# Kernel optimization log

Measured on AMD Instinct MI355X. Metric: run time of the kernel, lower is better.

The kernel has to match this reference:

```python
import jax, jax.numpy as jnp
import numpy as np

E = 64        # num_experts
T = 65536     # num_tokens (sum of group_sizes)
D_IN = 512    # in_features
D_OUT = 512   # out_features


def setup_inputs() -> dict:
    key = jax.random.key(0)
    k1, k2, k3 = jax.random.split(key, 3)
    inputs = jax.random.normal(k1, (T, D_IN), dtype=jnp.float32)
    # lecun_normal init scale for kernel
    kernel = jax.random.normal(k2, (E, D_IN, D_OUT), dtype=jnp.float32) * (1.0 / np.sqrt(D_IN))
    bias = jax.random.normal(k3, (D_OUT,), dtype=jnp.float32) * 0.02
    # equal-size contiguous per-expert token groups, summing to T
    group_sizes = jnp.full((E,), T // E, dtype=jnp.int32)
    return {"inputs": inputs, "kernel": kernel, "bias": bias, "group_sizes": group_sizes}


def reference(inputs, kernel, bias, group_sizes):
    # Grouped (ragged) matmul: tokens are laid out contiguously by expert;
    # group_sizes[e] tokens are multiplied by kernel[e]. This is exactly
    # jax.lax.ragged_dot (megablocks-style grouped GEMM semantics).
    y = jax.lax.ragged_dot(inputs, kernel, group_sizes)  # [T, D_OUT]
    return y + bias[None, :]
```

## Files before the change

kernel.cpp:

```cpp
#include <hip/hip_runtime.h>
#include <hip/hip_bf16.h>

#define NUM_E 64
#define D_K 512
#define D_N 512
#define BM 128
#define BN 128
#define MAX_TILES 576
#define GRID_X (MAX_TILES * 4)

typedef __bf16 bf16x8 __attribute__((ext_vector_type(8)));
typedef float f32x16 __attribute__((ext_vector_type(16)));
typedef float f32x4 __attribute__((ext_vector_type(4)));
typedef unsigned int u32;
typedef unsigned short u16;

__device__ __forceinline__ int imin(int a, int b) { return a < b ? a : b; }

__device__ __forceinline__ void gll16(const void* g, void* l) {
    __builtin_amdgcn_global_load_lds(
        (const __attribute__((address_space(1))) u32*)(uintptr_t)g,
        (__attribute__((address_space(3))) u32*)(uintptr_t)l, 16, 0, 0);
}

__device__ __forceinline__ void cvt_split(float a, u32 &hi, u32 &lo) {
    u32 u  = __float_as_uint(a);
    u32 rh = (u + 0x7FFFu + ((u >> 16) & 1u)) & 0xFFFF0000u;
    hi = rh >> 16;
    float res = a - __uint_as_float(rh);
    lo = __float_as_uint(res) >> 16;
}

__global__ void build_tiles_kernel(const int* __restrict__ gs,
                                   int* __restrict__ cnt,
                                   int* __restrict__ desc) {
    int e = threadIdx.x;
    if (e >= NUM_E) return;
    int row = 0, toff = 0;
    for (int i = 0; i < e; ++i) {
        int g = gs[i];
        row += g;
        toff += (g + BM - 1) / BM;
    }
    int g = gs[e];
    int nt = (g + BM - 1) / BM;
    for (int i = 0; i < nt; ++i) {
        int b = 3 * (toff + i);
        desc[b]     = e;
        desc[b + 1] = row + i * BM;
        desc[b + 2] = imin(BM, g - i * BM);
    }
    if (e == NUM_E - 1) cnt[0] = toff + nt;
}

__global__ void convert_x_kernel(const float* __restrict__ X, u16* __restrict__ Xc,
                                 int nquads) {
    int idx = blockIdx.x * blockDim.x + threadIdx.x;
    int stride = gridDim.x * blockDim.x;
    for (int q = idx; q < nquads; q += stride) {
        int row = q >> 7;
        int c4  = (q & 127) * 4;
        f32x4 v = *(const f32x4*)(X + (size_t)q * 4);
        u32 h[4], l[4];
        #pragma unroll
        for (int j = 0; j < 4; ++j) cvt_split(v[j], h[j], l[j]);
        uint2 hp, lp;
        hp.x = h[0] | (h[1] << 16); hp.y = h[2] | (h[3] << 16);
        lp.x = l[0] | (l[1] << 16); lp.y = l[2] | (l[3] << 16);
        *(uint2*)(Xc + (size_t)row * 1024 + c4)       = hp;
        *(uint2*)(Xc + (size_t)row * 1024 + 512 + c4) = lp;
    }
}

__global__ void convert_w_kernel(const float* __restrict__ W, u16* __restrict__ Wc) {
    __shared__ u16 Thi[64 * 68];
    __shared__ u16 Tlo[64 * 68];
    int bid = blockIdx.x;
    int e  = bid >> 6;
    int ti = (bid >> 3) & 7;
    int tj = bid & 7;
    int tid = threadIdx.x;

    const float* Wp = W + (size_t)e * D_K * D_N;
    #pragma unroll
    for (int it = 0; it < 4; ++it) {
        int kl = it * 16 + (tid >> 4);
        int nl = (tid & 15) * 4;
        f32x4 v = *(const f32x4*)(Wp + (size_t)(ti * 64 + kl) * D_N + tj * 64 + nl);
        u32 h[4], l[4];
        #pragma unroll
        for (int j = 0; j < 4; ++j) cvt_split(v[j], h[j], l[j]);
        uint2 hp, lp;
        hp.x = h[0] | (h[1] << 16); hp.y = h[2] | (h[3] << 16);
        lp.x = l[0] | (l[1] << 16); lp.y = l[2] | (l[3] << 16);
        *(uint2*)(Thi + kl * 68 + nl) = hp;
        *(uint2*)(Tlo + kl * 68 + nl) = lp;
    }
    __syncthreads();
    #pragma unroll
    for (int it = 0; it < 4; ++it) {
        int nl = it * 16 + (tid >> 4);
        int kq = tid & 15;
        u32 h[4], l[4];
        #pragma unroll
        for (int j = 0; j < 4; ++j) {
            h[j] = Thi[(kq * 4 + j) * 68 + nl];
            l[j] = Tlo[(kq * 4 + j) * 68 + nl];
        }
        uint2 hp, lp;
        hp.x = h[0] | (h[1] << 16); hp.y = h[2] | (h[3] << 16);
        lp.x = l[0] | (l[1] << 16); lp.y = l[2] | (l[3] << 16);
        u16* outp = Wc + ((size_t)e << 19) + (size_t)(tj * 64 + nl) * 1024 + ti * 64;
        *(uint2*)(outp + kq * 4)       = hp;
        *(uint2*)(outp + 512 + kq * 4) = lp;
    }
}

__global__ void __launch_bounds__(256, 3)
gemm_split_kernel(const u16* __restrict__ Xc, const u16* __restrict__ Wc,
                  const float* __restrict__ bias, const int* __restrict__ cnt,
                  const int* __restrict__ desc, float* __restrict__ out, int T) {
    __shared__ u16 As[BM * 64];
    __shared__ u16 Bs[BN * 64];

    int bid = blockIdx.x;
    int s = (bid & 7) * (GRID_X / 8) + (bid >> 3);
    int tile  = s >> 2;
    int ntile = s & 3;
    if (tile >= cnt[0]) return;

    int expert = desc[3 * tile];
    int row0   = desc[3 * tile + 1];
    int rows   = desc[3 * tile + 2];
    int n0 = ntile * BN;

    const int tid  = threadIdx.x;
    const int lane = tid & 63;
    const int wid  = tid >> 6;
    const int wm = wid >> 1, wn = wid & 1;
    const int lr = lane & 31, kg = lane >> 5;

    int aoff[4], boff[4], ldsb[4];
    #pragma unroll
    for (int c = 0; c < 4; ++c) {
        int chunk = c * 256 + tid;
        int r = chunk >> 3, j = chunk & 7;
        int cb = (j * 16) ^ ((r & 7) << 4);
        int ar = imin(row0 + r, T - 1);
        aoff[c] = ar * 1024 + (cb >> 1);
        boff[c] = (expert << 19) + (n0 + r) * 1024 + (cb >> 1);
        ldsb[c] = (c * 256 + wid * 64) * 16;
    }

    f32x16 acc[2][2];
    #pragma unroll
    for (int i = 0; i < 2; ++i)
        #pragma unroll
        for (int j = 0; j < 2; ++j)
            #pragma unroll
            for (int r = 0; r < 16; ++r) acc[i][j][r] = 0.0f;

    for (int t = 0; t < 24; ++t) {
        int tt = t & 7, seg = t >> 3;
        int acol = tt * 64 + (seg == 2 ? 512 : 0);
        int bcol = tt * 64 + (seg == 1 ? 512 : 0);
        #pragma unroll
        for (int c = 0; c < 4; ++c) {
            gll16(Xc + aoff[c] + acol, (char*)As + ldsb[c]);
            gll16(Wc + boff[c] + bcol, (char*)Bs + ldsb[c]);
        }
        __syncthreads();

        #pragma unroll
        for (int ks = 0; ks < 4; ++ks) {
            int kb = ks * 32 + kg * 16;
            bf16x8 af[2], bb[2];
            #pragma unroll
            for (int f = 0; f < 2; ++f) {
                int ra = wm * 64 + f * 32 + lr;
                af[f] = *(const bf16x8*)((const char*)As + ra * 128 + (kb ^ ((ra & 7) << 4)));
                int rb = wn * 64 + f * 32 + lr;
                bb[f] = *(const bf16x8*)((const char*)Bs + rb * 128 + (kb ^ ((rb & 7) << 4)));
            }
            #pragma unroll
            for (int i = 0; i < 2; ++i)
                #pragma unroll
                for (int j = 0; j < 2; ++j)
                    acc[i][j] = __builtin_amdgcn_mfma_f32_32x32x16_bf16(af[i], bb[j], acc[i][j], 0, 0, 0);
        }
        __syncthreads();
    }

    #pragma unroll
    for (int j = 0; j < 2; ++j) {
        int col = n0 + wn * 64 + j * 32 + lr;
        float bv = bias[col];
        #pragma unroll
        for (int i = 0; i < 2; ++i) {
            #pragma unroll
            for (int r = 0; r < 16; ++r) {
                int lm = wm * 64 + i * 32 + (r & 3) + 8 * (r >> 2) + 4 * kg;
                if (lm < rows)
                    out[(size_t)(row0 + lm) * D_N + col] = acc[i][j][r] + bv;
            }
        }
    }
}

#define KPAD 72
__global__ void __launch_bounds__(256, 2)
grouped_gemm_fallback(const float* __restrict__ X, const float* __restrict__ W,
                      const float* __restrict__ bias, const int* __restrict__ cnt,
                      const int* __restrict__ desc, float* __restrict__ out) {
    extern __shared__ u16 lds[];
    u16* Ahi = lds;
    u16* Alo = Ahi + BM * KPAD;
    u16* Bhi = Alo + BM * KPAD;
    u16* Blo = Bhi + BM * KPAD;

    int bid = blockIdx.x;
    int s = (bid & 7) * (GRID_X / 8) + (bid >> 3);
    int tile  = s >> 2;
    int ntile = s & 3;
    if (tile >= cnt[0]) return;

    int expert = desc[3 * tile];
    int row0   = desc[3 * tile + 1];
    int rows   = desc[3 * tile + 2];
    int n0 = ntile * BN;

    const int tid  = threadIdx.x;
    const int lane = tid & 63;
    const int wid  = tid >> 6;
    const int wm = wid >> 1, wn = wid & 1;
    const int lr = lane & 31, kg = lane >> 5;

    const float* Wp = W + (size_t)expert * D_K * D_N;

    f32x16 acc[2][2];
    #pragma unroll
    for (int i = 0; i < 2; ++i)
        #pragma unroll
        for (int j = 0; j < 2; ++j)
            #pragma unroll
            for (int r = 0; r < 16; ++r) acc[i][j][r] = 0.0f;

    for (int kt = 0; kt < D_K / 64; ++kt) {
        int k0 = kt * 64;
        #pragma unroll
        for (int it = 0; it < 8; ++it) {
            int idx = it * 256 + tid;
            int m = idx >> 4, q = idx & 15;
            f32x4 v;
            if (m < rows) v = *(const f32x4*)(X + (size_t)(row0 + m) * D_K + k0 + q * 4);
            else          v[0] = v[1] = v[2] = v[3] = 0.0f;
            u32 h[4], l[4];
            #pragma unroll
            for (int j = 0; j < 4; ++j) cvt_split(v[j], h[j], l[j]);
            uint2 hp, lp;
            hp.x = h[0] | (h[1] << 16); hp.y = h[2] | (h[3] << 16);
            lp.x = l[0] | (l[1] << 16); lp.y = l[2] | (l[3] << 16);
            *(uint2*)(Ahi + m * KPAD + q * 4) = hp;
            *(uint2*)(Alo + m * KPAD + q * 4) = lp;
        }
        #pragma unroll
        for (int it = 0; it < 8; ++it) {
            int idx = it * 256 + tid;
            int n = idx & 127, kb = idx >> 7;
            const float* bp = Wp + (size_t)(k0 + kb * 4) * D_N + n0 + n;
            u32 h[4], l[4];
            #pragma unroll
            for (int j = 0; j < 4; ++j) { float b = bp[(size_t)j * D_N]; cvt_split(b, h[j], l[j]); }
            uint2 hp, lp;
            hp.x = h[0] | (h[1] << 16); hp.y = h[2] | (h[3] << 16);
            lp.x = l[0] | (l[1] << 16); lp.y = l[2] | (l[3] << 16);
            *(uint2*)(Bhi + n * KPAD + kb * 4) = hp;
            *(uint2*)(Blo + n * KPAD + kb * 4) = lp;
        }
        __syncthreads();
        #pragma unroll
        for (int ks = 0; ks < 4; ++ks) {
            bf16x8 ah[2], al[2], bh[2], bl[2];
            #pragma unroll
            for (int f = 0; f < 2; ++f) {
                int aoff2 = (wm * 64 + f * 32 + lr) * KPAD + ks * 16 + kg * 8;
                ah[f] = *(const bf16x8*)(Ahi + aoff2);
                al[f] = *(const bf16x8*)(Alo + aoff2);
                int boff2 = (wn * 64 + f * 32 + lr) * KPAD + ks * 16 + kg * 8;
                bh[f] = *(const bf16x8*)(Bhi + boff2);
                bl[f] = *(const bf16x8*)(Blo + boff2);
            }
            #pragma unroll
            for (int i = 0; i < 2; ++i)
                #pragma unroll
                for (int j = 0; j < 2; ++j) {
                    acc[i][j] = __builtin_amdgcn_mfma_f32_32x32x16_bf16(ah[i], bh[j], acc[i][j], 0, 0, 0);
                    acc[i][j] = __builtin_amdgcn_mfma_f32_32x32x16_bf16(ah[i], bl[j], acc[i][j], 0, 0, 0);
                    acc[i][j] = __builtin_amdgcn_mfma_f32_32x32x16_bf16(al[i], bh[j], acc[i][j], 0, 0, 0);
                }
        }
        __syncthreads();
    }
    #pragma unroll
    for (int j = 0; j < 2; ++j) {
        int col = n0 + wn * 64 + j * 32 + lr;
        float bv = bias[col];
        #pragma unroll
        for (int i = 0; i < 2; ++i) {
            #pragma unroll
            for (int r = 0; r < 16; ++r) {
                int lm = wm * 64 + i * 32 + (r & 3) + 8 * (r >> 2) + 4 * kg;
                if (lm < rows)
                    out[(size_t)(row0 + lm) * D_N + col] = acc[i][j][r] + bv;
            }
        }
    }
}

extern "C" void kernel_launch(void* const* d_in, const int* in_sizes, int n_in,
                              void* d_out, int out_size, void* d_ws, size_t ws_size,
                              hipStream_t stream) {
    const float* X    = (const float*)d_in[0];
    const float* W    = (const float*)d_in[1];
    const float* bias = (const float*)d_in[2];
    const int*   gs   = (const int*)d_in[3];
    float* out = (float*)d_out;

    int T = in_sizes[0] / D_K;

    int* cnt  = (int*)d_ws;
    int* desc = cnt + 4;
    hipLaunchKernelGGL(build_tiles_kernel, dim3(1), dim3(64), 0, stream, gs, cnt, desc);

    size_t x_bytes = (size_t)T * 1024 * sizeof(u16);
    size_t w_bytes = (size_t)NUM_E * D_N * 1024 * sizeof(u16);
    size_t need = 8192 + x_bytes + w_bytes;

    if (ws_size >= need) {
        u16* Xc = (u16*)((char*)d_ws + 8192);
        u16* Wc = (u16*)((char*)d_ws + 8192 + x_bytes);

        int nquads = T * (D_K / 4);
        hipLaunchKernelGGL(convert_x_kernel, dim3(4096), dim3(256), 0, stream, X, Xc, nquads);
        hipLaunchKernelGGL(convert_w_kernel, dim3(NUM_E * 64), dim3(256), 0, stream, W, Wc);
        hipLaunchKernelGGL(gemm_split_kernel, dim3(GRID_X), dim3(256), 0, stream,
                           Xc, Wc, bias, cnt, desc, out, T);
    } else {
        const size_t lds_bytes = (size_t)4 * BM * KPAD * sizeof(u16);
        hipLaunchKernelGGL(grouped_gemm_fallback, dim3(GRID_X), dim3(256), lds_bytes, stream,
                           X, W, bias, cnt, desc, out);
    }
}
```

Baseline: 460.8 us.

## Double-buffer LDS tiles in split-bf16 GEMM and widen conversion stores

The GEMM main loop now uses two LDS buffers and issues the global-to-LDS loads for the next K step before computing on the current one. It waits with explicit vmcnt counts and raw barriers instead of a full sync before and after every step, so load latency can overlap MFMA work. The X and W conversion kernels now handle eight elements per thread with 16-byte stores, and the W transpose stages raw floats in LDS. Doubling LDS use forces launch bounds down from 3 to 2 blocks per CU, which reduces occupancy.

```diff
diff --git a/kernel.cpp b/kernel.cpp
--- a/kernel.cpp
+++ b/kernel.cpp
@@ -54,74 +54,76 @@
 }
 
 __global__ void convert_x_kernel(const float* __restrict__ X, u16* __restrict__ Xc,
-                                 int nquads) {
+                                 int nocts) {
     int idx = blockIdx.x * blockDim.x + threadIdx.x;
     int stride = gridDim.x * blockDim.x;
-    for (int q = idx; q < nquads; q += stride) {
-        int row = q >> 7;
-        int c4  = (q & 127) * 4;
-        f32x4 v = *(const f32x4*)(X + (size_t)q * 4);
-        u32 h[4], l[4];
-        #pragma unroll
-        for (int j = 0; j < 4; ++j) cvt_split(v[j], h[j], l[j]);
-        uint2 hp, lp;
+    for (int o = idx; o < nocts; o += stride) {
+        int row = o >> 6;
+        int c8  = (o & 63) * 8;
+        const float* p = X + (size_t)o * 8;
+        f32x4 v0 = *(const f32x4*)p;
+        f32x4 v1 = *(const f32x4*)(p + 4);
+        u32 h[8], l[8];
+        #pragma unroll
+        for (int j = 0; j < 4; ++j) cvt_split(v0[j], h[j], l[j]);
+        #pragma unroll
+        for (int j = 0; j < 4; ++j) cvt_split(v1[j], h[4 + j], l[4 + j]);
+        uint4 hp, lp;
         hp.x = h[0] | (h[1] << 16); hp.y = h[2] | (h[3] << 16);
+        hp.z = h[4] | (h[5] << 16); hp.w = h[6] | (h[7] << 16);
         lp.x = l[0] | (l[1] << 16); lp.y = l[2] | (l[3] << 16);
-        *(uint2*)(Xc + (size_t)row * 1024 + c4)       = hp;
-        *(uint2*)(Xc + (size_t)row * 1024 + 512 + c4) = lp;
+        lp.z = l[4] | (l[5] << 16); lp.w = l[6] | (l[7] << 16);
+        *(uint4*)(Xc + (size_t)row * 1024 + c8)       = hp;
+        *(uint4*)(Xc + (size_t)row * 1024 + 512 + c8) = lp;
     }
 }
 
 __global__ void convert_w_kernel(const float* __restrict__ W, u16* __restrict__ Wc) {
-    __shared__ u16 Thi[64 * 68];
-    __shared__ u16 Tlo[64 * 68];
+    __shared__ float Tf[64 * 68];
     int bid = blockIdx.x;
     int e  = bid >> 6;
     int ti = (bid >> 3) & 7;
     int tj = bid & 7;
     int tid = threadIdx.x;
 
-    const float* Wp = W + (size_t)e * D_K * D_N;
+    const float* Wp = W + (size_t)e * D_K * D_N + (size_t)(ti * 64) * D_N + tj * 64;
     #pragma unroll
     for (int it = 0; it < 4; ++it) {
         int kl = it * 16 + (tid >> 4);
         int nl = (tid & 15) * 4;
-        f32x4 v = *(const f32x4*)(Wp + (size_t)(ti * 64 + kl) * D_N + tj * 64 + nl);
-        u32 h[4], l[4];
-        #pragma unroll
-        for (int j = 0; j < 4; ++j) cvt_split(v[j], h[j], l[j]);
-        uint2 hp, lp;
+        f32x4 v = *(const f32x4*)(Wp + (size_t)kl * D_N + nl);
+        #pragma unroll
+        for (int j = 0; j < 4; ++j) Tf[(nl + j) * 68 + kl] = v[j];
+    }
+    __syncthreads();
+    #pragma unroll
+    for (int it = 0; it < 2; ++it) {
+        int nl = it * 32 + (tid >> 3);
+        int ko = (tid & 7) * 8;
+        f32x4 a = *(const f32x4*)(Tf + nl * 68 + ko);
+        f32x4 b = *(const f32x4*)(Tf + nl * 68 + ko + 4);
+        u32 h[8], l[8];
+        #pragma unroll
+        for (int j = 0; j < 4; ++j) cvt_split(a[j], h[j], l[j]);
+        #pragma unroll
+        for (int j = 0; j < 4; ++j) cvt_split(b[j], h[4 + j], l[4 + j]);
+        uint4 hp, lp;
         hp.x = h[0] | (h[1] << 16); hp.y = h[2] | (h[3] << 16);
+        hp.z = h[4] | (h[5] << 16); hp.w = h[6] | (h[7] << 16);
         lp.x = l[0] | (l[1] << 16); lp.y = l[2] | (l[3] << 16);
-        *(uint2*)(Thi + kl * 68 + nl) = hp;
-        *(uint2*)(Tlo + kl * 68 + nl) = lp;
-    }
-    __syncthreads();
-    #pragma unroll
-    for (int it = 0; it < 4; ++it) {
-        int nl = it * 16 + (tid >> 4);
-        int kq = tid & 15;
-        u32 h[4], l[4];
-        #pragma unroll
-        for (int j = 0; j < 4; ++j) {
-            h[j] = Thi[(kq * 4 + j) * 68 + nl];
-            l[j] = Tlo[(kq * 4 + j) * 68 + nl];
-        }
-        uint2 hp, lp;
-        hp.x = h[0] | (h[1] << 16); hp.y = h[2] | (h[3] << 16);
-        lp.x = l[0] | (l[1] << 16); lp.y = l[2] | (l[3] << 16);
-        u16* outp = Wc + ((size_t)e << 19) + (size_t)(tj * 64 + nl) * 1024 + ti * 64;
-        *(uint2*)(outp + kq * 4)       = hp;
-        *(uint2*)(outp + 512 + kq * 4) = lp;
-    }
-}
-
-__global__ void __launch_bounds__(256, 3)
+        lp.z = l[4] | (l[5] << 16); lp.w = l[6] | (l[7] << 16);
+        u16* outp = Wc + ((size_t)e << 19) + (size_t)(tj * 64 + nl) * 1024 + ti * 64 + ko;
+        *(uint4*)outp         = hp;
+        *(uint4*)(outp + 512) = lp;
+    }
+}
+
+__global__ void __launch_bounds__(256, 2)
 gemm_split_kernel(const u16* __restrict__ Xc, const u16* __restrict__ Wc,
                   const float* __restrict__ bias, const int* __restrict__ cnt,
                   const int* __restrict__ desc, float* __restrict__ out, int T) {
-    __shared__ u16 As[BM * 64];
-    __shared__ u16 Bs[BN * 64];
+    __shared__ u16 As[2][BM * 64];
+    __shared__ u16 Bs[2][BN * 64];
 
     int bid = blockIdx.x;
     int s = (bid & 7) * (GRID_X / 8) + (bid >> 3);
@@ -160,17 +162,33 @@
             #pragma unroll
             for (int r = 0; r < 16; ++r) acc[i][j][r] = 0.0f;
 
+    #pragma unroll
+    for (int c = 0; c < 4; ++c) {
+        gll16(Xc + aoff[c], (char*)As[0] + ldsb[c]);
+        gll16(Wc + boff[c], (char*)Bs[0] + ldsb[c]);
+    }
+
     for (int t = 0; t < 24; ++t) {
-        int tt = t & 7, seg = t >> 3;
-        int acol = tt * 64 + (seg == 2 ? 512 : 0);
-        int bcol = tt * 64 + (seg == 1 ? 512 : 0);
-        #pragma unroll
-        for (int c = 0; c < 4; ++c) {
-            gll16(Xc + aoff[c] + acol, (char*)As + ldsb[c]);
-            gll16(Wc + boff[c] + bcol, (char*)Bs + ldsb[c]);
-        }
-        __syncthreads();
-
+        int cur = t & 1;
+        if (t < 23) {
+            int tn  = t + 1;
+            int tt  = tn & 7, seg = tn >> 3;
+            int acol = tt * 64 + (seg == 2 ? 512 : 0);
+            int bcol = tt * 64 + (seg == 1 ? 512 : 0);
+            int nxt = cur ^ 1;
+            #pragma unroll
+            for (int c = 0; c < 4; ++c) {
+                gll16(Xc + aoff[c] + acol, (char*)As[nxt] + ldsb[c]);
+                gll16(Wc + boff[c] + bcol, (char*)Bs[nxt] + ldsb[c]);
+            }
+            asm volatile("s_waitcnt vmcnt(8)" ::: "memory");
+        } else {
+            asm volatile("s_waitcnt vmcnt(0)" ::: "memory");
+        }
+        __builtin_amdgcn_s_barrier();
+
+        const char* Ab = (const char*)As[cur];
+        const char* Bb = (const char*)Bs[cur];
         #pragma unroll
         for (int ks = 0; ks < 4; ++ks) {
             int kb = ks * 32 + kg * 16;
@@ -178,9 +196,9 @@
             #pragma unroll
             for (int f = 0; f < 2; ++f) {
                 int ra = wm * 64 + f * 32 + lr;
-                af[f] = *(const bf16x8*)((const char*)As + ra * 128 + (kb ^ ((ra & 7) << 4)));
+                af[f] = *(const bf16x8*)(Ab + ra * 128 + (kb ^ ((ra & 7) << 4)));
                 int rb = wn * 64 + f * 32 + lr;
-                bb[f] = *(const bf16x8*)((const char*)Bs + rb * 128 + (kb ^ ((rb & 7) << 4)));
+                bb[f] = *(const bf16x8*)(Bb + rb * 128 + (kb ^ ((rb & 7) << 4)));
             }
             #pragma unroll
             for (int i = 0; i < 2; ++i)
@@ -188,7 +206,8 @@
                 for (int j = 0; j < 2; ++j)
                     acc[i][j] = __builtin_amdgcn_mfma_f32_32x32x16_bf16(af[i], bb[j], acc[i][j], 0, 0, 0);
         }
-        __syncthreads();
+        asm volatile("" ::: "memory");
+        __builtin_amdgcn_s_barrier();
     }
 
     #pragma unroll
@@ -340,8 +359,8 @@
         u16* Xc = (u16*)((char*)d_ws + 8192);
         u16* Wc = (u16*)((char*)d_ws + 8192 + x_bytes);
 
-        int nquads = T * (D_K / 4);
-        hipLaunchKernelGGL(convert_x_kernel, dim3(4096), dim3(256), 0, stream, X, Xc, nquads);
+        int nocts = T * (D_K / 8);
+        hipLaunchKernelGGL(convert_x_kernel, dim3(2048), dim3(256), 0, stream, X, Xc, nocts);
         hipLaunchKernelGGL(convert_w_kernel, dim3(NUM_E * 64), dim3(256), 0, stream, W, Wc);
         hipLaunchKernelGGL(gemm_split_kernel, dim3(GRID_X), dim3(256), 0, stream,
                            Xc, Wc, bias, cnt, desc, out, T);
```

Result: no change. 463.4 us (+0.6%).
